# Performance work log

Measured on AMD Instinct MI355X. Metric: run time of the kernel, lower is better.

Reference implementation:

```python
import jax, jax.numpy as jnp
import numpy as np

B, S, D, H, F = 4, 2048, 256, 8, 2  # batch, seq, input_size, heads, mlp factor
EPS = 1e-5


def _ln(x, g, b):
    m = jnp.mean(x, axis=-1, keepdims=True)
    v = jnp.var(x, axis=-1, keepdims=True)
    return (x - m) / jnp.sqrt(v + EPS) * g + b


def setup_inputs() -> dict:
    key = jax.random.key(0)
    ks = jax.random.split(key, 12)
    s = 1.0 / np.sqrt(D)
    return {
        "X":  jax.random.normal(ks[0], (B, S, D), jnp.float32),
        # Wide attention: each of H heads has full [D,D] Q/K/V projections (no bias)
        "Wq": jax.random.uniform(ks[1], (H, D, D), jnp.float32, -s, s),
        "Wk": jax.random.uniform(ks[2], (H, D, D), jnp.float32, -s, s),
        "Wv": jax.random.uniform(ks[3], (H, D, D), jnp.float32, -s, s),
        "Wz": jax.random.uniform(ks[4], (H * D, D), jnp.float32, -1.0 / np.sqrt(H * D), 1.0 / np.sqrt(H * D)),
        "bz": jnp.zeros((D,), jnp.float32),
        "W1": jax.random.uniform(ks[5], (D, F * D), jnp.float32, -s, s),
        "b1": jnp.zeros((F * D,), jnp.float32),
        "W2": jax.random.uniform(ks[6], (F * D, D), jnp.float32, -1.0 / np.sqrt(F * D), 1.0 / np.sqrt(F * D)),
        "b2": jnp.zeros((D,), jnp.float32),
        "g1": jnp.ones((D,), jnp.float32),
        "be1": jnp.zeros((D,), jnp.float32),
        "g2": jnp.ones((D,), jnp.float32),
        "be2": jnp.zeros((D,), jnp.float32),
    }


def reference(X, Wq, Wk, Wv, Wz, bz, W1, b1, W2, b2, g1, be1, g2, be2):
    scale = D ** (-0.25)  # applied to both q and k as in the source
    q = jnp.einsum('bsd,hde->hbse', X, Wq) * scale   # [H,B,S,D]
    k = jnp.einsum('btd,hde->hbte', X, Wk) * scale
    v = jnp.einsum('btd,hde->hbte', X, Wv)
    attn = jax.nn.softmax(jnp.einsum('hbse,hbte->hbst', q, k), axis=-1)  # [H,B,S,S]
    zh = jnp.einsum('hbst,hbte->hbse', attn, v)       # [H,B,S,D]
    # concat heads along feature dim (head order matters for Wz)
    zcat = jnp.transpose(zh, (1, 2, 0, 3)).reshape(B, S, H * D)
    z = zcat @ Wz + bz
    z = _ln(z + X, g1, be1)                            # dropout p=0 -> identity
    z_ff = jnp.maximum(z @ W1 + b1, 0.0) @ W2 + b2
    z = _ln(z_ff + z, g2, be2)
    attn_mean = jnp.mean(attn, axis=0)                 # [B,S,S]
    return z, attn_mean
```

## Files before the change

kernel.cpp:

```cpp
#include <hip/hip_runtime.h>
#include <cstdint>
#include <cstddef>

#define B_  4
#define S_  2048
#define D_  256
#define H_  8
#define FD_ 512
#define N_  (B_*S_)
#define HD_ (H_*D_)
#define EPS 1e-5f

typedef __attribute__((ext_vector_type(8))) short bf16x8;
typedef __attribute__((ext_vector_type(8))) unsigned short u16x8;
typedef __attribute__((ext_vector_type(4))) float f32x4;

__device__ __forceinline__ unsigned short f2bf(float f) {
  union { float f; unsigned u; } x; x.f = f;
  unsigned u = x.u;
  return (unsigned short)((u + 0x7FFFu + ((u >> 16) & 1u)) >> 16);
}
__device__ __forceinline__ float bf2f(unsigned short h) {
  union { unsigned u; float f; } x; x.u = ((unsigned)h) << 16; return x.f;
}

__device__ __forceinline__ void glds16(const void* gptr, void* ldsptr) {
  __builtin_amdgcn_global_load_lds(
      (__attribute__((address_space(1))) void*)gptr,
      (__attribute__((address_space(3))) void*)ldsptr,
      16, 0, 0);
}

__device__ __forceinline__ int sw32(int row, int u) {
  return (row*32 + ((u & 24) | ((u & 7) ^ (row & 7)))) * 8;
}
__device__ __forceinline__ int sw16(int row, int u) {
  return (row*16 + ((u & 8) | ((u & 7) ^ (row & 7)))) * 8;
}

__global__ __launch_bounds__(256) void cast_x_kernel(
    const float* __restrict__ X, unsigned short* __restrict__ Xb)
{
  const size_t i8 = ((size_t)blockIdx.x * 256 + threadIdx.x) * 8;
  float4 a = *(const float4*)&X[i8];
  float4 b = *(const float4*)&X[i8 + 4];
  u16x8 o;
  o[0]=f2bf(a.x); o[1]=f2bf(a.y); o[2]=f2bf(a.z); o[3]=f2bf(a.w);
  o[4]=f2bf(b.x); o[5]=f2bf(b.y); o[6]=f2bf(b.z); o[7]=f2bf(b.w);
  *(u16x8*)&Xb[i8] = o;
}

__global__ __launch_bounds__(256) void prep_w_kernel(
    const float* __restrict__ Wq, const float* __restrict__ Wk,
    const float* __restrict__ Wv, unsigned short* __restrict__ Wt)
{
  __shared__ float tile[64][65];
  const int tid = threadIdx.x;
  const int d0 = blockIdx.x * 64, e0 = blockIdx.y * 64;
  const int w = blockIdx.z;
  const float* src;
  float scale;
  if (w < 8)       { src = Wq + (size_t)w*D_*D_;      scale = 0.25f; }
  else if (w < 16) { src = Wk + (size_t)(w-8)*D_*D_;  scale = 0.25f; }
  else             { src = Wv + (size_t)(w-16)*D_*D_; scale = 1.0f;  }
  {
    int r = tid >> 2, c16 = (tid & 3) * 16;
    const float* s = src + (size_t)(d0 + r)*D_ + e0 + c16;
    #pragma unroll
    for (int u = 0; u < 4; ++u) *(float4*)&tile[r][c16 + u*4] = *(const float4*)(s + u*4);
  }
  __syncthreads();
  {
    int er = tid >> 2, dc = (tid & 3) * 16;
    u16x8 o0, o1;
    #pragma unroll
    for (int j = 0; j < 8; ++j) {
      o0[j] = f2bf(tile[dc + j][er] * scale);
      o1[j] = f2bf(tile[dc + 8 + j][er] * scale);
    }
    unsigned short* dst = Wt + ((size_t)w*D_ + e0 + er)*D_ + d0 + dc;
    *(u16x8*)(dst)     = o0;
    *(u16x8*)(dst + 8) = o1;
  }
}

__global__ __launch_bounds__(256) void tcast_kernel(
    const float* __restrict__ src, unsigned short* __restrict__ dst,
    int R, int C)
{
  __shared__ float tile[64][65];
  const int tid = threadIdx.x;
  const int r0 = blockIdx.x * 64, c0 = blockIdx.y * 64;
  {
    int r = tid >> 2, c16 = (tid & 3) * 16;
    const float* s = src + (size_t)(r0 + r)*C + c0 + c16;
    #pragma unroll
    for (int u = 0; u < 4; ++u) *(float4*)&tile[r][c16 + u*4] = *(const float4*)(s + u*4);
  }
  __syncthreads();
  {
    int cr = tid >> 2, rc = (tid & 3) * 16;
    u16x8 o0, o1;
    #pragma unroll
    for (int j = 0; j < 8; ++j) {
      o0[j] = f2bf(tile[rc + j][cr]);
      o1[j] = f2bf(tile[rc + 8 + j][cr]);
    }
    unsigned short* d = dst + (size_t)(c0 + cr)*R + r0 + rc;
    *(u16x8*)(d)     = o0;
    *(u16x8*)(d + 8) = o1;
  }
}

__global__ __launch_bounds__(256) void qkv_kernel(
    const unsigned short* __restrict__ Xb, const unsigned short* __restrict__ Wt,
    unsigned short* __restrict__ q, unsigned short* __restrict__ k,
    unsigned short* __restrict__ v)
{
  __shared__ unsigned short Xt[64*32*8];
  __shared__ unsigned short Wtile[64*32*8];
  const int tid = threadIdx.x;
  const int w4 = tid >> 6, lane = tid & 63;
  const int c = lane & 15, qd = lane >> 4;
  const int n0 = blockIdx.x * 64;
  const int e0 = blockIdx.y * 64;
  const int w  = blockIdx.z;

  unsigned short* obase;
  if (w < 8)       obase = q + (size_t)w*N_*D_;
  else if (w < 16) obase = k + (size_t)(w-8)*N_*D_;
  else             obase = v + (size_t)(w-16)*N_*D_;

  {
    const char* xg = (const char*)Xb + (size_t)n0*512;
    const char* wg = (const char*)Wt + ((size_t)w*D_ + e0)*512;
    #pragma unroll
    for (int i = 0; i < 8; ++i) {
      int g = w4*8 + i;
      int r = 2*g + (lane >> 5);
      int su = lane & 31;
      int u = (su & 24) | ((su & 7) ^ (r & 7));
      glds16(xg + (size_t)r*512 + u*16, &Xt[g*512]);
      glds16(wg + (size_t)r*512 + u*16, &Wtile[g*512]);
    }
  }
  __syncthreads();

  f32x4 sc[4];
  #pragma unroll
  for (int nc = 0; nc < 4; ++nc) sc[nc] = (f32x4){0.f,0.f,0.f,0.f};
  #pragma unroll
  for (int ks = 0; ks < 8; ++ks) {
    bf16x8 xa = *(const bf16x8*)&Xt[sw32(16*w4 + c, ks*4 + qd)];
    #pragma unroll
    for (int nc = 0; nc < 4; ++nc) {
      bf16x8 bf = *(const bf16x8*)&Wtile[sw32(nc*16 + c, ks*4 + qd)];
      sc[nc] = __builtin_amdgcn_mfma_f32_16x16x32_bf16(xa, bf, sc[nc], 0, 0, 0);
    }
  }
  #pragma unroll
  for (int nc = 0; nc < 4; ++nc)
    #pragma unroll
    for (int r = 0; r < 4; ++r)
      obase[(size_t)(n0 + 16*w4 + qd*4 + r)*D_ + e0 + nc*16 + c] = f2bf(sc[nc][r]);
}

__global__ __launch_bounds__(256) void vtrans_kernel(
    const unsigned short* __restrict__ vb, unsigned short* __restrict__ vT)
{
  __shared__ unsigned short tile[64][72];
  const int tid = threadIdx.x;
  const int t0 = blockIdx.x * 64, e0 = blockIdx.y * 64;
  const int h = blockIdx.z >> 2, b = blockIdx.z & 3;
  const size_t in_base = (size_t)h*N_*D_ + (size_t)b*S_*D_;
  {
    int r = tid >> 2, c16 = (tid & 3) * 16;
    const unsigned short* src = vb + in_base + (size_t)(t0 + r)*D_ + e0 + c16;
    *(u16x8*)&tile[r][c16]     = *(const u16x8*)(src);
    *(u16x8*)&tile[r][c16 + 8] = *(const u16x8*)(src + 8);
  }
  __syncthreads();
  {
    int er = tid >> 2, tt = (tid & 3) * 16;
    u16x8 o0, o1;
    #pragma unroll
    for (int j = 0; j < 8; ++j) { o0[j] = tile[tt+j][er]; o1[j] = tile[tt+8+j][er]; }
    unsigned short* dst = vT + ((size_t)(h*4 + b)*D_ + e0 + er)*S_ + t0 + tt;
    *(u16x8*)(dst)     = o0;
    *(u16x8*)(dst + 8) = o1;
  }
}

__global__ __launch_bounds__(256, 2) void attn_ol_kernel(
    const unsigned short* __restrict__ qb, const unsigned short* __restrict__ kb,
    const unsigned short* __restrict__ vT, unsigned short* __restrict__ zcatb,
    float* __restrict__ Lws)
{
  __shared__ unsigned short Kt[2][32*32*8];
  __shared__ unsigned short Vt[2][16*544];
  const int tid = threadIdx.x;
  const int w = tid >> 6, lane = tid & 63;
  const int c = lane & 15, qd = lane >> 4;
  const int wg = blockIdx.x;
  const int xcd = wg & 7;
  const int slot = wg >> 3;
  const int j = slot & 15;
  const int gg = slot >> 4;
  const int g = gg*8 + xcd;
  const int h = g >> 2, b = g & 3;
  const int s0 = j * 128;

  const size_t qkbase = (size_t)h*N_*D_ + (size_t)b*S_*D_;

  bf16x8 qa[2][8];
  #pragma unroll
  for (int mi = 0; mi < 2; ++mi) {
    const unsigned short* qrow = qb + qkbase + (size_t)(s0 + 32*w + 16*mi + c)*D_ + qd*8;
    #pragma unroll
    for (int ks = 0; ks < 8; ++ks) qa[mi][ks] = *(const bf16x8*)(qrow + ks*32);
  }

  f32x4 o[2][16];
  #pragma unroll
  for (int mi = 0; mi < 2; ++mi)
    #pragma unroll
    for (int i = 0; i < 16; ++i) o[mi][i] = (f32x4){0.f,0.f,0.f,0.f};
  float Lp[2] = {0.f, 0.f};

  const char* kB = (const char*)(kb + qkbase);
  const char* vB = (const char*)(vT + (size_t)(h*4 + b)*D_*S_);

  #define STAGE_OL(kt_, bi_)                                                   \
    {                                                                          \
      _Pragma("unroll")                                                        \
      for (int i = 0; i < 4; ++i) {                                            \
        int gq = w*4 + i;                                                      \
        int r = 2*gq + (lane >> 5);                                            \
        int Lg = ((r >> 2) & 3)*8 + (r >> 4)*4 + (r & 3);                      \
        int su = lane & 31;                                                    \
        int u = (su & 24) | ((su & 7) ^ (r & 7));                              \
        glds16(kB + ((size_t)(kt_)*32 + Lg)*512 + u*16, &Kt[bi_][gq*512]);     \
      }                                                                        \
      _Pragma("unroll")                                                        \
      for (int i = 0; i < 4; ++i) {                                            \
        int gq = w*4 + i;                                                      \
        int e = gq*16 + (lane >> 2);                                           \
        int qv = (lane & 3) ^ ((lane >> 3) & 3);                               \
        glds16(vB + (size_t)e*4096 + (size_t)(kt_)*64 + qv*16, &Vt[bi_][gq*544]);\
      }                                                                        \
    }

  STAGE_OL(0, 0);

  for (int kt = 0; kt < 64; ++kt) {
    const int bi = kt & 1;
    __syncthreads();
    if (kt + 1 < 64) STAGE_OL(kt + 1, bi ^ 1);

    f32x4 sc[2][2];
    #pragma unroll
    for (int mi = 0; mi < 2; ++mi)
      #pragma unroll
      for (int nc = 0; nc < 2; ++nc) sc[mi][nc] = (f32x4){0.f,0.f,0.f,0.f};
    #pragma unroll
    for (int ks = 0; ks < 8; ++ks) {
      bf16x8 kf0 = *(const bf16x8*)&Kt[bi][sw32(c,      ks*4 + qd)];
      bf16x8 kf1 = *(const bf16x8*)&Kt[bi][sw32(16 + c, ks*4 + qd)];
      #pragma unroll
      for (int mi = 0; mi < 2; ++mi) {
        sc[mi][0] = __builtin_amdgcn_mfma_f32_16x16x32_bf16(kf0, qa[mi][ks], sc[mi][0], 0, 0, 0);
        sc[mi][1] = __builtin_amdgcn_mfma_f32_16x16x32_bf16(kf1, qa[mi][ks], sc[mi][1], 0, 0, 0);
      }
    }
    bf16x8 pa[2];
    #pragma unroll
    for (int mi = 0; mi < 2; ++mi) {
      float ex[2][4];
      #pragma unroll
      for (int nc = 0; nc < 2; ++nc)
        #pragma unroll
        for (int r = 0; r < 4; ++r) {
          float p = __expf(sc[mi][nc][r]);
          ex[nc][r] = p;
          Lp[mi] += p;
        }
      union { unsigned u[4]; bf16x8 v; } cv;
      asm("v_cvt_pk_bf16_f32 %0, %1, %2" : "=v"(cv.u[0]) : "v"(ex[0][0]), "v"(ex[0][1]));
      asm("v_cvt_pk_bf16_f32 %0, %1, %2" : "=v"(cv.u[1]) : "v"(ex[0][2]), "v"(ex[0][3]));
      asm("v_cvt_pk_bf16_f32 %0, %1, %2" : "=v"(cv.u[2]) : "v"(ex[1][0]), "v"(ex[1][1]));
      asm("v_cvt_pk_bf16_f32 %0, %1, %2" : "=v"(cv.u[3]) : "v"(ex[1][2]), "v"(ex[1][3]));
      pa[mi] = cv.v;
    }
    #pragma unroll
    for (int ec = 0; ec < 16; ++ec) {
      bf16x8 vf = *(const bf16x8*)&Vt[bi][ec*544 + c*32 + (qd ^ ((c >> 1) & 3))*8];
      o[0][ec] = __builtin_amdgcn_mfma_f32_16x16x32_bf16(pa[0], vf, o[0][ec], 0, 0, 0);
      o[1][ec] = __builtin_amdgcn_mfma_f32_16x16x32_bf16(pa[1], vf, o[1][ec], 0, 0, 0);
    }
  }

  #pragma unroll
  for (int mi = 0; mi < 2; ++mi) {
    float L = Lp[mi];
    L += __shfl_xor(L, 16);
    L += __shfl_xor(L, 32);
    if (qd == 0)
      Lws[(size_t)h*N_ + b*S_ + s0 + 32*w + 16*mi + c] = L;
    float il[4];
    #pragma unroll
    for (int r = 0; r < 4; ++r)
      il[r] = 1.0f / __shfl(L, (lane & 48) | (qd*4 + r));
    #pragma unroll
    for (int ec = 0; ec < 16; ++ec)
      #pragma unroll
      for (int r = 0; r < 4; ++r)
        zcatb[(size_t)(b*S_ + s0 + 32*w + 16*mi + qd*4 + r)*HD_ + h*D_ + ec*16 + c] =
            f2bf(o[mi][ec][r] * il[r]);
  }
  #undef STAGE_OL
}

__global__ __launch_bounds__(256, 2) void attn_mean_kernel(
    const unsigned short* __restrict__ qb, const unsigned short* __restrict__ kb,
    const float* __restrict__ Lws, float* __restrict__ out_attn)
{
  __shared__ unsigned short Kt[2][64*32*8];
  const int tid = threadIdx.x;
  const int w = tid >> 6, lane = tid & 63;
  const int c = lane & 15, qd = lane >> 4;
  const int wg = blockIdx.x;
  const int xcd = wg & 7;
  const int slot = wg >> 3;
  const int j = slot & 15;
  const int ggg = slot >> 4;
  const int g = ggg*8 + xcd;
  const int b = g >> 5;
  const int t0 = (g & 31) * 64;
  const int s0 = j * 128;

  float am[2][4][4] = {};

  #define STAGE_AM(h_, bi_)                                                    \
    {                                                                          \
      const char* kB = (const char*)(kb + (size_t)(h_)*N_*D_ + (size_t)b*S_*D_);\
      _Pragma("unroll")                                                        \
      for (int i = 0; i < 8; ++i) {                                            \
        int gq = w*8 + i;                                                      \
        int r = 2*gq + (lane >> 5);                                            \
        int su = lane & 31;                                                    \
        int u = (su & 24) | ((su & 7) ^ (r & 7));                              \
        glds16(kB + ((size_t)t0 + r)*512 + u*16, &Kt[bi_][gq*512]);            \
      }                                                                        \
    }

  STAGE_AM(0, 0);

  bf16x8 qa[2][8];
  #pragma unroll
  for (int mi = 0; mi < 2; ++mi) {
    const unsigned short* qrow = qb + (size_t)b*S_*D_ + (size_t)(s0 + 32*w + 16*mi + c)*D_ + qd*8;
    #pragma unroll
    for (int ks = 0; ks < 8; ++ks) qa[mi][ks] = *(const bf16x8*)(qrow + ks*32);
  }

  for (int h = 0; h < 8; ++h) {
    const int bi = h & 1;
    __syncthreads();
    if (h + 1 < 8) STAGE_AM(h + 1, bi ^ 1);

    float il[2][4];
    #pragma unroll
    for (int mi = 0; mi < 2; ++mi)
      #pragma unroll
      for (int r = 0; r < 4; ++r)
        il[mi][r] = 0.125f / Lws[(size_t)h*N_ + b*S_ + s0 + 32*w + 16*mi + qd*4 + r];

    bf16x8 qn[2][8];
    if (h + 1 < 8) {
      const size_t basen = (size_t)(h+1)*N_*D_ + (size_t)b*S_*D_;
      #pragma unroll
      for (int mi = 0; mi < 2; ++mi) {
        const unsigned short* qrow = qb + basen + (size_t)(s0 + 32*w + 16*mi + c)*D_ + qd*8;
        #pragma unroll
        for (int ks = 0; ks < 8; ++ks) qn[mi][ks] = *(const bf16x8*)(qrow + ks*32);
      }
    }

    f32x4 sc[2][4];
    #pragma unroll
    for (int mi = 0; mi < 2; ++mi)
      #pragma unroll
      for (int nc = 0; nc < 4; ++nc) sc[mi][nc] = (f32x4){0.f,0.f,0.f,0.f};
    #pragma unroll
    for (int ks = 0; ks < 8; ++ks) {
      #pragma unroll
      for (int nc = 0; nc < 4; ++nc) {
        bf16x8 kf = *(const bf16x8*)&Kt[bi][sw32(nc*16 + c, ks*4 + qd)];
        sc[0][nc] = __builtin_amdgcn_mfma_f32_16x16x32_bf16(qa[0][ks], kf, sc[0][nc], 0, 0, 0);
        sc[1][nc] = __builtin_amdgcn_mfma_f32_16x16x32_bf16(qa[1][ks], kf, sc[1][nc], 0, 0, 0);
      }
    }
    #pragma unroll
    for (int mi = 0; mi < 2; ++mi)
      #pragma unroll
      for (int nc = 0; nc < 4; ++nc)
        #pragma unroll
        for (int r = 0; r < 4; ++r)
          am[mi][nc][r] += __expf(sc[mi][nc][r]) * il[mi][r];

    if (h + 1 < 8) {
      #pragma unroll
      for (int mi = 0; mi < 2; ++mi)
        #pragma unroll
        for (int ks = 0; ks < 8; ++ks) qa[mi][ks] = qn[mi][ks];
    }
  }
  #pragma unroll
  for (int mi = 0; mi < 2; ++mi)
    #pragma unroll
    for (int nc = 0; nc < 4; ++nc)
      #pragma unroll
      for (int r = 0; r < 4; ++r)
        out_attn[(size_t)(b*S_ + s0 + 32*w + 16*mi + qd*4 + r)*S_ + t0 + nc*16 + c] =
            am[mi][nc][r];
  #undef STAGE_AM
}

__global__ __launch_bounds__(256) void wz_ln1_kernel(
    const unsigned short* __restrict__ zcatb, const unsigned short* __restrict__ Wzt,
    const float* __restrict__ bz, const float* __restrict__ X,
    const float* __restrict__ g1, const float* __restrict__ be1,
    unsigned short* __restrict__ z1b)
{
  __shared__ unsigned short At[32*16*8];
  __shared__ unsigned short Wt2[256*16*8];
  __shared__ float redS[2][32], redQ[2][32];
  const int tid = threadIdx.x;
  const int w4 = tid >> 6, lane = tid & 63;
  const int c = lane & 15, qd = lane >> 4;
  const int n0 = blockIdx.x * 32;
  const int msub = w4 & 1, ehalf = w4 >> 1;

  f32x4 acc[8];
  #pragma unroll
  for (int nc = 0; nc < 8; ++nc) acc[nc] = (f32x4){0.f,0.f,0.f,0.f};

  for (int kc = 0; kc < 16; ++kc) {
    {
      const char* ab = (const char*)zcatb + (size_t)n0*4096 + (size_t)kc*256;
      #pragma unroll
      for (int i = 0; i < 2; ++i) {
        int g = w4*2 + i;
        int r = g*4 + (lane >> 4);
        int su = lane & 15;
        int u = (su & 8) | ((su & 7) ^ (r & 7));
        glds16(ab + (size_t)r*4096 + u*16, &At[g*512]);
      }
      const char* wb = (const char*)Wzt + (size_t)kc*256;
      #pragma unroll
      for (int i = 0; i < 16; ++i) {
        int g = w4*16 + i;
        int e = g*4 + (lane >> 4);
        int su = lane & 15;
        int u = (su & 8) | ((su & 7) ^ (e & 7));
        glds16(wb + (size_t)e*4096 + u*16, &Wt2[g*512]);
      }
    }
    __syncthreads();
    #pragma unroll
    for (int ks = 0; ks < 4; ++ks) {
      bf16x8 a = *(const bf16x8*)&At[sw16(msub*16 + c, ks*4 + qd)];
      #pragma unroll
      for (int nc = 0; nc < 8; ++nc) {
        bf16x8 bv = *(const bf16x8*)&Wt2[sw16(ehalf*128 + nc*16 + c, ks*4 + qd)];
        acc[nc] = __builtin_amdgcn_mfma_f32_16x16x32_bf16(a, bv, acc[nc], 0, 0, 0);
      }
    }
    __syncthreads();
  }

  float vals[8][4];
  float sum_[4] = {0.f,0.f,0.f,0.f}, sq_[4] = {0.f,0.f,0.f,0.f};
  #pragma unroll
  for (int nc = 0; nc < 8; ++nc) {
    int e = ehalf*128 + nc*16 + c;
    #pragma unroll
    for (int r = 0; r < 4; ++r) {
      int n = n0 + msub*16 + qd*4 + r;
      float v = acc[nc][r] + bz[e] + X[(size_t)n*D_ + e];
      vals[nc][r] = v;
      sum_[r] += v; sq_[r] += v*v;
    }
  }
  #pragma unroll
  for (int off = 1; off < 16; off <<= 1) {
    #pragma unroll
    for (int r = 0; r < 4; ++r) {
      sum_[r] += __shfl_xor(sum_[r], off);
      sq_[r]  += __shfl_xor(sq_[r],  off);
    }
  }
  if (c == 0) {
    #pragma unroll
    for (int r = 0; r < 4; ++r) {
      redS[ehalf][msub*16 + qd*4 + r] = sum_[r];
      redQ[ehalf][msub*16 + qd*4 + r] = sq_[r];
    }
  }
  __syncthreads();
  #pragma unroll
  for (int r = 0; r < 4; ++r) {
    int lr = msub*16 + qd*4 + r;
    float Sv = redS[0][lr] + redS[1][lr];
    float Qv = redQ[0][lr] + redQ[1][lr];
    float mean = Sv * (1.0f/D_);
    float var  = Qv * (1.0f/D_) - mean*mean;
    float rstd = rsqrtf(var + EPS);
    int n = n0 + lr;
    #pragma unroll
    for (int nc = 0; nc < 8; ++nc) {
      int e = ehalf*128 + nc*16 + c;
      z1b[(size_t)n*D_ + e] = f2bf((vals[nc][r] - mean)*rstd*g1[e] + be1[e]);
    }
  }
}

__global__ __launch_bounds__(256) void mlp1_kernel(
    const unsigned short* __restrict__ z1b, const unsigned short* __restrict__ W1t,
    const float* __restrict__ b1, unsigned short* __restrict__ hbuf)
{
  __shared__ unsigned short At[64*32*8];
  __shared__ unsigned short Bt[64*32*8];
  const int tid = threadIdx.x;
  const int w4 = tid >> 6, lane = tid & 63;
  const int c = lane & 15, qd = lane >> 4;
  const int n0 = blockIdx.x * 64;
  const int f0 = blockIdx.y * 64;

  {
    const char* ag = (const char*)z1b + (size_t)n0*512;
    const char* bg = (const char*)W1t + (size_t)f0*512;
    #pragma unroll
    for (int i = 0; i < 8; ++i) {
      int g = w4*8 + i;
      int r = 2*g + (lane >> 5);
      int su = lane & 31;
      int u = (su & 24) | ((su & 7) ^ (r & 7));
      glds16(ag + (size_t)r*512 + u*16, &At[g*512]);
      glds16(bg + (size_t)r*512 + u*16, &Bt[g*512]);
    }
  }
  __syncthreads();

  f32x4 sc[4];
  #pragma unroll
  for (int nc = 0; nc < 4; ++nc) sc[nc] = (f32x4){0.f,0.f,0.f,0.f};
  #pragma unroll
  for (int ks = 0; ks < 8; ++ks) {
    bf16x8 xa = *(const bf16x8*)&At[sw32(16*w4 + c, ks*4 + qd)];
    #pragma unroll
    for (int nc = 0; nc < 4; ++nc) {
      bf16x8 bf = *(const bf16x8*)&Bt[sw32(nc*16 + c, ks*4 + qd)];
      sc[nc] = __builtin_amdgcn_mfma_f32_16x16x32_bf16(xa, bf, sc[nc], 0, 0, 0);
    }
  }
  #pragma unroll
  for (int nc = 0; nc < 4; ++nc) {
    int f = f0 + nc*16 + c;
    float bias = b1[f];
    #pragma unroll
    for (int r = 0; r < 4; ++r)
      hbuf[(size_t)(n0 + 16*w4 + qd*4 + r)*FD_ + f] = f2bf(fmaxf(sc[nc][r] + bias, 0.f));
  }
}

__global__ __launch_bounds__(256) void mlp2_kernel(
    const unsigned short* __restrict__ hbuf, const unsigned short* __restrict__ W2t,
    const float* __restrict__ b2, const unsigned short* __restrict__ z1b,
    const float* __restrict__ g2, const float* __restrict__ be2,
    float* __restrict__ out)
{
  __shared__ unsigned short At[32*16*8];
  __shared__ unsigned short Wt2[256*16*8];
  __shared__ float redS[2][32], redQ[2][32];
  const int tid = threadIdx.x;
  const int w4 = tid >> 6, lane = tid & 63;
  const int c = lane & 15, qd = lane >> 4;
  const int n0 = blockIdx.x * 32;
  const int msub = w4 & 1, ehalf = w4 >> 1;

  f32x4 acc[8];
  #pragma unroll
  for (int nc = 0; nc < 8; ++nc) acc[nc] = (f32x4){0.f,0.f,0.f,0.f};

  for (int kc = 0; kc < 4; ++kc) {
    {
      const char* ab = (const char*)hbuf + (size_t)n0*1024 + (size_t)kc*256;
      #pragma unroll
      for (int i = 0; i < 2; ++i) {
        int g = w4*2 + i;
        int r = g*4 + (lane >> 4);
        int su = lane & 15;
        int u = (su & 8) | ((su & 7) ^ (r & 7));
        glds16(ab + (size_t)r*1024 + u*16, &At[g*512]);
      }
      const char* wb = (const char*)W2t + (size_t)kc*256;
      #pragma unroll
      for (int i = 0; i < 16; ++i) {
        int g = w4*16 + i;
        int e = g*4 + (lane >> 4);
        int su = lane & 15;
        int u = (su & 8) | ((su & 7) ^ (e & 7));
        glds16(wb + (size_t)e*1024 + u*16, &Wt2[g*512]);
      }
    }
    __syncthreads();
    #pragma unroll
    for (int ks = 0; ks < 4; ++ks) {
      bf16x8 a = *(const bf16x8*)&At[sw16(msub*16 + c, ks*4 + qd)];
      #pragma unroll
      for (int nc = 0; nc < 8; ++nc) {
        bf16x8 bv = *(const bf16x8*)&Wt2[sw16(ehalf*128 + nc*16 + c, ks*4 + qd)];
        acc[nc] = __builtin_amdgcn_mfma_f32_16x16x32_bf16(a, bv, acc[nc], 0, 0, 0);
      }
    }
    __syncthreads();
  }

  float vals[8][4];
  float sum_[4] = {0.f,0.f,0.f,0.f}, sq_[4] = {0.f,0.f,0.f,0.f};
  #pragma unroll
  for (int nc = 0; nc < 8; ++nc) {
    int e = ehalf*128 + nc*16 + c;
    #pragma unroll
    for (int r = 0; r < 4; ++r) {
      int n = n0 + msub*16 + qd*4 + r;
      float v = acc[nc][r] + b2[e] + bf2f(z1b[(size_t)n*D_ + e]);
      vals[nc][r] = v;
      sum_[r] += v; sq_[r] += v*v;
    }
  }
  #pragma unroll
  for (int off = 1; off < 16; off <<= 1) {
    #pragma unroll
    for (int r = 0; r < 4; ++r) {
      sum_[r] += __shfl_xor(sum_[r], off);
      sq_[r]  += __shfl_xor(sq_[r],  off);
    }
  }
  if (c == 0) {
    #pragma unroll
    for (int r = 0; r < 4; ++r) {
      redS[ehalf][msub*16 + qd*4 + r] = sum_[r];
      redQ[ehalf][msub*16 + qd*4 + r] = sq_[r];
    }
  }
  __syncthreads();
  #pragma unroll
  for (int r = 0; r < 4; ++r) {
    int lr = msub*16 + qd*4 + r;
    float Sv = redS[0][lr] + redS[1][lr];
    float Qv = redQ[0][lr] + redQ[1][lr];
    float mean = Sv * (1.0f/D_);
    float var  = Qv * (1.0f/D_) - mean*mean;
    float rstd = rsqrtf(var + EPS);
    int n = n0 + lr;
    #pragma unroll
    for (int nc = 0; nc < 8; ++nc) {
      int e = ehalf*128 + nc*16 + c;
      out[(size_t)n*D_ + e] = (vals[nc][r] - mean)*rstd*g2[e] + be2[e];
    }
  }
}

extern "C" void kernel_launch(void* const* d_in, const int* in_sizes, int n_in,
                              void* d_out, int out_size, void* d_ws, size_t ws_size,
                              hipStream_t stream)
{
  (void)in_sizes; (void)n_in; (void)out_size; (void)ws_size;
  const float* X   = (const float*)d_in[0];
  const float* Wq  = (const float*)d_in[1];
  const float* Wk  = (const float*)d_in[2];
  const float* Wv  = (const float*)d_in[3];
  const float* Wz  = (const float*)d_in[4];
  const float* bz  = (const float*)d_in[5];
  const float* W1  = (const float*)d_in[6];
  const float* b1  = (const float*)d_in[7];
  const float* W2  = (const float*)d_in[8];
  const float* b2  = (const float*)d_in[9];
  const float* g1  = (const float*)d_in[10];
  const float* be1 = (const float*)d_in[11];
  const float* g2  = (const float*)d_in[12];
  const float* be2 = (const float*)d_in[13];

  char* p = (char*)d_ws;
  unsigned short* Xbb  = (unsigned short*)p; p += (size_t)N_*D_*2;
  unsigned short* Wtb  = (unsigned short*)p; p += (size_t)24*D_*D_*2;
  unsigned short* Wztb = (unsigned short*)p; p += (size_t)D_*HD_*2;
  unsigned short* W1tb = (unsigned short*)p; p += (size_t)FD_*D_*2;
  unsigned short* W2tb = (unsigned short*)p; p += (size_t)D_*FD_*2;
  unsigned short* qbuf = (unsigned short*)p; p += (size_t)H_*N_*D_*2;
  unsigned short* kbuf = (unsigned short*)p; p += (size_t)H_*N_*D_*2;
  unsigned short* vbuf = (unsigned short*)p; p += (size_t)H_*N_*D_*2;
  unsigned short* vTb  = (unsigned short*)p; p += (size_t)H_*N_*D_*2;
  float* Lws   = (float*)p; p += (size_t)H_*N_*4;
  unsigned short* zcatb = (unsigned short*)p; p += (size_t)N_*HD_*2;
  unsigned short* z1b   = (unsigned short*)p; p += (size_t)N_*D_*2;
  unsigned short* hbuf  = (unsigned short*)p;

  float* out_z    = (float*)d_out;
  float* out_attn = out_z + (size_t)N_*D_;

  cast_x_kernel<<<N_*D_/(256*8), 256, 0, stream>>>(X, Xbb);

  dim3 gW(4, 4, 24);
  prep_w_kernel<<<gW, 256, 0, stream>>>(Wq, Wk, Wv, Wtb);

  { dim3 g(HD_/64, D_/64);  tcast_kernel<<<g, 256, 0, stream>>>(Wz, Wztb, HD_, D_); }
  { dim3 g(D_/64, FD_/64);  tcast_kernel<<<g, 256, 0, stream>>>(W1, W1tb, D_, FD_); }
  { dim3 g(FD_/64, D_/64);  tcast_kernel<<<g, 256, 0, stream>>>(W2, W2tb, FD_, D_); }

  dim3 gA(N_/64, D_/64, 24);
  qkv_kernel<<<gA, 256, 0, stream>>>(Xbb, Wtb, qbuf, kbuf, vbuf);

  dim3 gT(S_/64, D_/64, H_*B_);
  vtrans_kernel<<<gT, 256, 0, stream>>>(vbuf, vTb);

  attn_ol_kernel<<<512, 256, 0, stream>>>(qbuf, kbuf, vTb, zcatb, Lws);

  attn_mean_kernel<<<2048, 256, 0, stream>>>(qbuf, kbuf, Lws, out_attn);

  wz_ln1_kernel<<<N_/32, 256, 0, stream>>>(zcatb, Wztb, bz, X, g1, be1, z1b);

  dim3 gM1(N_/64, FD_/64);
  mlp1_kernel<<<gM1, 256, 0, stream>>>(z1b, W1tb, b1, hbuf);

  mlp2_kernel<<<N_/32, 256, 0, stream>>>(hbuf, W2tb, b2, z1b, g2, be2, out_z);
}
```

Measured before the change: 533.8 us.

## Load K and Q fragments directly from global memory instead of LDS staging

```diff
diff --git a/kernel.cpp b/kernel.cpp
--- a/kernel.cpp
+++ b/kernel.cpp
@@ -196,7 +196,6 @@
     const unsigned short* __restrict__ vT, unsigned short* __restrict__ zcatb,
     float* __restrict__ Lws)
 {
-  __shared__ unsigned short Kt[2][32*32*8];
   __shared__ unsigned short Vt[2][16*544];
   const int tid = threadIdx.x;
   const int w = tid >> 6, lane = tid & 63;
@@ -230,17 +229,11 @@
   const char* kB = (const char*)(kb + qkbase);
   const char* vB = (const char*)(vT + (size_t)(h*4 + b)*D_*S_);
 
+  const int rowb0 = (((c >> 2) & 3)*8 + (c & 3))*512 + qd*16;
+  const int rowb1 = rowb0 + 4*512;
+
   #define STAGE_OL(kt_, bi_)                                                   \
     {                                                                          \
-      _Pragma("unroll")                                                        \
-      for (int i = 0; i < 4; ++i) {                                            \
-        int gq = w*4 + i;                                                      \
-        int r = 2*gq + (lane >> 5);                                            \
-        int Lg = ((r >> 2) & 3)*8 + (r >> 4)*4 + (r & 3);                      \
-        int su = lane & 31;                                                    \
-        int u = (su & 24) | ((su & 7) ^ (r & 7));                              \
-        glds16(kB + ((size_t)(kt_)*32 + Lg)*512 + u*16, &Kt[bi_][gq*512]);     \
-      }                                                                        \
       _Pragma("unroll")                                                        \
       for (int i = 0; i < 4; ++i) {                                            \
         int gq = w*4 + i;                                                      \
@@ -257,6 +250,7 @@
     __syncthreads();
     if (kt + 1 < 64) STAGE_OL(kt + 1, bi ^ 1);
 
+    const char* ktb = kB + (size_t)kt*16384;
     f32x4 sc[2][2];
     #pragma unroll
     for (int mi = 0; mi < 2; ++mi)
@@ -264,8 +258,8 @@
       for (int nc = 0; nc < 2; ++nc) sc[mi][nc] = (f32x4){0.f,0.f,0.f,0.f};
     #pragma unroll
     for (int ks = 0; ks < 8; ++ks) {
-      bf16x8 kf0 = *(const bf16x8*)&Kt[bi][sw32(c,      ks*4 + qd)];
-      bf16x8 kf1 = *(const bf16x8*)&Kt[bi][sw32(16 + c, ks*4 + qd)];
+      bf16x8 kf0 = *(const bf16x8*)(ktb + rowb0 + ks*64);
+      bf16x8 kf1 = *(const bf16x8*)(ktb + rowb1 + ks*64);
       #pragma unroll
       for (int mi = 0; mi < 2; ++mi) {
         sc[mi][0] = __builtin_amdgcn_mfma_f32_16x16x32_bf16(kf0, qa[mi][ks], sc[mi][0], 0, 0, 0);
@@ -320,11 +314,10 @@
   #undef STAGE_OL
 }
 
-__global__ __launch_bounds__(256, 2) void attn_mean_kernel(
+__global__ __launch_bounds__(256, 4) void attn_mean_kernel(
     const unsigned short* __restrict__ qb, const unsigned short* __restrict__ kb,
     const float* __restrict__ Lws, float* __restrict__ out_attn)
 {
-  __shared__ unsigned short Kt[2][64*32*8];
   const int tid = threadIdx.x;
   const int w = tid >> 6, lane = tid & 63;
   const int c = lane & 15, qd = lane >> 4;
@@ -340,33 +333,13 @@
 
   float am[2][4][4] = {};
 
-  #define STAGE_AM(h_, bi_)                                                    \
-    {                                                                          \
-      const char* kB = (const char*)(kb + (size_t)(h_)*N_*D_ + (size_t)b*S_*D_);\
-      _Pragma("unroll")                                                        \
-      for (int i = 0; i < 8; ++i) {                                            \
-        int gq = w*8 + i;                                                      \
-        int r = 2*gq + (lane >> 5);                                            \
-        int su = lane & 31;                                                    \
-        int u = (su & 24) | ((su & 7) ^ (r & 7));                              \
-        glds16(kB + ((size_t)t0 + r)*512 + u*16, &Kt[bi_][gq*512]);            \
-      }                                                                        \
-    }
-
-  STAGE_AM(0, 0);
-
-  bf16x8 qa[2][8];
-  #pragma unroll
-  for (int mi = 0; mi < 2; ++mi) {
-    const unsigned short* qrow = qb + (size_t)b*S_*D_ + (size_t)(s0 + 32*w + 16*mi + c)*D_ + qd*8;
-    #pragma unroll
-    for (int ks = 0; ks < 8; ++ks) qa[mi][ks] = *(const bf16x8*)(qrow + ks*32);
-  }
+  const char* qBase = (const char*)qb + ((size_t)b*S_ + s0 + 32*w + c)*512 + qd*16;
+  const char* kBase = (const char*)kb + ((size_t)b*S_ + t0 + c)*512 + qd*16;
 
   for (int h = 0; h < 8; ++h) {
-    const int bi = h & 1;
-    __syncthreads();
-    if (h + 1 < 8) STAGE_AM(h + 1, bi ^ 1);
+    const size_t hoff = (size_t)h*N_*D_*2;
+    const char* qh = qBase + hoff;
+    const char* kh = kBase + hoff;
 
     float il[2][4];
     #pragma unroll
@@ -375,17 +348,6 @@
       for (int r = 0; r < 4; ++r)
         il[mi][r] = 0.125f / Lws[(size_t)h*N_ + b*S_ + s0 + 32*w + 16*mi + qd*4 + r];
 
-    bf16x8 qn[2][8];
-    if (h + 1 < 8) {
-      const size_t basen = (size_t)(h+1)*N_*D_ + (size_t)b*S_*D_;
-      #pragma unroll
-      for (int mi = 0; mi < 2; ++mi) {
-        const unsigned short* qrow = qb + basen + (size_t)(s0 + 32*w + 16*mi + c)*D_ + qd*8;
-        #pragma unroll
-        for (int ks = 0; ks < 8; ++ks) qn[mi][ks] = *(const bf16x8*)(qrow + ks*32);
-      }
-    }
-
     f32x4 sc[2][4];
     #pragma unroll
     for (int mi = 0; mi < 2; ++mi)
@@ -393,11 +355,13 @@
       for (int nc = 0; nc < 4; ++nc) sc[mi][nc] = (f32x4){0.f,0.f,0.f,0.f};
     #pragma unroll
     for (int ks = 0; ks < 8; ++ks) {
+      bf16x8 qa0 = *(const bf16x8*)(qh + ks*64);
+      bf16x8 qa1 = *(const bf16x8*)(qh + 16*512 + ks*64);
       #pragma unroll
       for (int nc = 0; nc < 4; ++nc) {
-        bf16x8 kf = *(const bf16x8*)&Kt[bi][sw32(nc*16 + c, ks*4 + qd)];
-        sc[0][nc] = __builtin_amdgcn_mfma_f32_16x16x32_bf16(qa[0][ks], kf, sc[0][nc], 0, 0, 0);
-        sc[1][nc] = __builtin_amdgcn_mfma_f32_16x16x32_bf16(qa[1][ks], kf, sc[1][nc], 0, 0, 0);
+        bf16x8 kf = *(const bf16x8*)(kh + nc*16*512 + ks*64);
+        sc[0][nc] = __builtin_amdgcn_mfma_f32_16x16x32_bf16(qa0, kf, sc[0][nc], 0, 0, 0);
+        sc[1][nc] = __builtin_amdgcn_mfma_f32_16x16x32_bf16(qa1, kf, sc[1][nc], 0, 0, 0);
       }
     }
     #pragma unroll
@@ -407,13 +371,6 @@
         #pragma unroll
         for (int r = 0; r < 4; ++r)
           am[mi][nc][r] += __expf(sc[mi][nc][r]) * il[mi][r];
-
-    if (h + 1 < 8) {
-      #pragma unroll
-      for (int mi = 0; mi < 2; ++mi)
-        #pragma unroll
-        for (int ks = 0; ks < 8; ++ks) qa[mi][ks] = qn[mi][ks];
-    }
   }
   #pragma unroll
   for (int mi = 0; mi < 2; ++mi)
@@ -423,7 +380,6 @@
       for (int r = 0; r < 4; ++r)
         out_attn[(size_t)(b*S_ + s0 + 32*w + 16*mi + qd*4 + r)*S_ + t0 + nc*16 + c] =
             am[mi][nc][r];
-  #undef STAGE_AM
 }
 
 __global__ __launch_bounds__(256) void wz_ln1_kernel(
```

Result: slower. 881.6 us (+65.2%).

## Single-buffer K tile and drop Q prefetch in attn_mean to raise occupancy

Applied to the files above, without the earlier changes.

```diff
diff --git a/kernel.cpp b/kernel.cpp
--- a/kernel.cpp
+++ b/kernel.cpp
@@ -320,11 +320,11 @@
   #undef STAGE_OL
 }
 
-__global__ __launch_bounds__(256, 2) void attn_mean_kernel(
+__global__ __launch_bounds__(256, 4) void attn_mean_kernel(
     const unsigned short* __restrict__ qb, const unsigned short* __restrict__ kb,
     const float* __restrict__ Lws, float* __restrict__ out_attn)
 {
-  __shared__ unsigned short Kt[2][64*32*8];
+  __shared__ unsigned short Kt[64*32*8];
   const int tid = threadIdx.x;
   const int w = tid >> 6, lane = tid & 63;
   const int c = lane & 15, qd = lane >> 4;
@@ -340,7 +340,7 @@
 
   float am[2][4][4] = {};
 
-  #define STAGE_AM(h_, bi_)                                                    \
+  #define STAGE_AM(h_)                                                         \
     {                                                                          \
       const char* kB = (const char*)(kb + (size_t)(h_)*N_*D_ + (size_t)b*S_*D_);\
       _Pragma("unroll")                                                        \
@@ -349,25 +349,21 @@
         int r = 2*gq + (lane >> 5);                                            \
         int su = lane & 31;                                                    \
         int u = (su & 24) | ((su & 7) ^ (r & 7));                              \
-        glds16(kB + ((size_t)t0 + r)*512 + u*16, &Kt[bi_][gq*512]);            \
+        glds16(kB + ((size_t)t0 + r)*512 + u*16, &Kt[gq*512]);                 \
       }                                                                        \
     }
 
-  STAGE_AM(0, 0);
-
-  bf16x8 qa[2][8];
-  #pragma unroll
-  for (int mi = 0; mi < 2; ++mi) {
-    const unsigned short* qrow = qb + (size_t)b*S_*D_ + (size_t)(s0 + 32*w + 16*mi + c)*D_ + qd*8;
-    #pragma unroll
-    for (int ks = 0; ks < 8; ++ks) qa[mi][ks] = *(const bf16x8*)(qrow + ks*32);
-  }
+  STAGE_AM(0);
 
   for (int h = 0; h < 8; ++h) {
-    const int bi = h & 1;
-    __syncthreads();
-    if (h + 1 < 8) STAGE_AM(h + 1, bi ^ 1);
-
+    bf16x8 qa[2][8];
+    const size_t base = (size_t)h*N_*D_ + (size_t)b*S_*D_;
+    #pragma unroll
+    for (int mi = 0; mi < 2; ++mi) {
+      const unsigned short* qrow = qb + base + (size_t)(s0 + 32*w + 16*mi + c)*D_ + qd*8;
+      #pragma unroll
+      for (int ks = 0; ks < 8; ++ks) qa[mi][ks] = *(const bf16x8*)(qrow + ks*32);
+    }
     float il[2][4];
     #pragma unroll
     for (int mi = 0; mi < 2; ++mi)
@@ -375,16 +371,7 @@
       for (int r = 0; r < 4; ++r)
         il[mi][r] = 0.125f / Lws[(size_t)h*N_ + b*S_ + s0 + 32*w + 16*mi + qd*4 + r];
 
-    bf16x8 qn[2][8];
-    if (h + 1 < 8) {
-      const size_t basen = (size_t)(h+1)*N_*D_ + (size_t)b*S_*D_;
-      #pragma unroll
-      for (int mi = 0; mi < 2; ++mi) {
-        const unsigned short* qrow = qb + basen + (size_t)(s0 + 32*w + 16*mi + c)*D_ + qd*8;
-        #pragma unroll
-        for (int ks = 0; ks < 8; ++ks) qn[mi][ks] = *(const bf16x8*)(qrow + ks*32);
-      }
-    }
+    __syncthreads();
 
     f32x4 sc[2][4];
     #pragma unroll
@@ -395,11 +382,17 @@
     for (int ks = 0; ks < 8; ++ks) {
       #pragma unroll
       for (int nc = 0; nc < 4; ++nc) {
-        bf16x8 kf = *(const bf16x8*)&Kt[bi][sw32(nc*16 + c, ks*4 + qd)];
+        bf16x8 kf = *(const bf16x8*)&Kt[sw32(nc*16 + c, ks*4 + qd)];
         sc[0][nc] = __builtin_amdgcn_mfma_f32_16x16x32_bf16(qa[0][ks], kf, sc[0][nc], 0, 0, 0);
         sc[1][nc] = __builtin_amdgcn_mfma_f32_16x16x32_bf16(qa[1][ks], kf, sc[1][nc], 0, 0, 0);
       }
     }
+
+    if (h + 1 < 8) {
+      __syncthreads();
+      STAGE_AM(h + 1);
+    }
+
     #pragma unroll
     for (int mi = 0; mi < 2; ++mi)
       #pragma unroll
@@ -407,13 +400,6 @@
         #pragma unroll
         for (int r = 0; r < 4; ++r)
           am[mi][nc][r] += __expf(sc[mi][nc][r]) * il[mi][r];
-
-    if (h + 1 < 8) {
-      #pragma unroll
-      for (int mi = 0; mi < 2; ++mi)
-        #pragma unroll
-        for (int ks = 0; ks < 8; ++ks) qa[mi][ks] = qn[mi][ks];
-    }
   }
   #pragma unroll
   for (int mi = 0; mi < 2; ++mi)
```

Result: slower. 699.2 us (+31.0%).

## Merge attention-mean and Wz+LayerNorm kernels into one branch-dispatched launch

Applied to the files above, without the earlier changes.

```diff
diff --git a/kernel.cpp b/kernel.cpp
--- a/kernel.cpp
+++ b/kernel.cpp
@@ -320,207 +320,208 @@
   #undef STAGE_OL
 }
 
-__global__ __launch_bounds__(256, 2) void attn_mean_kernel(
+#define FATSMEM (73728 + 512)
+__global__ __launch_bounds__(256, 2) void attn_mean_wz_kernel(
     const unsigned short* __restrict__ qb, const unsigned short* __restrict__ kb,
-    const float* __restrict__ Lws, float* __restrict__ out_attn)
-{
-  __shared__ unsigned short Kt[2][64*32*8];
-  const int tid = threadIdx.x;
-  const int w = tid >> 6, lane = tid & 63;
-  const int c = lane & 15, qd = lane >> 4;
-  const int wg = blockIdx.x;
-  const int xcd = wg & 7;
-  const int slot = wg >> 3;
-  const int j = slot & 15;
-  const int ggg = slot >> 4;
-  const int g = ggg*8 + xcd;
-  const int b = g >> 5;
-  const int t0 = (g & 31) * 64;
-  const int s0 = j * 128;
-
-  float am[2][4][4] = {};
-
-  #define STAGE_AM(h_, bi_)                                                    \
-    {                                                                          \
-      const char* kB = (const char*)(kb + (size_t)(h_)*N_*D_ + (size_t)b*S_*D_);\
-      _Pragma("unroll")                                                        \
-      for (int i = 0; i < 8; ++i) {                                            \
-        int gq = w*8 + i;                                                      \
-        int r = 2*gq + (lane >> 5);                                            \
-        int su = lane & 31;                                                    \
-        int u = (su & 24) | ((su & 7) ^ (r & 7));                              \
-        glds16(kB + ((size_t)t0 + r)*512 + u*16, &Kt[bi_][gq*512]);            \
-      }                                                                        \
-    }
-
-  STAGE_AM(0, 0);
-
-  bf16x8 qa[2][8];
-  #pragma unroll
-  for (int mi = 0; mi < 2; ++mi) {
-    const unsigned short* qrow = qb + (size_t)b*S_*D_ + (size_t)(s0 + 32*w + 16*mi + c)*D_ + qd*8;
-    #pragma unroll
-    for (int ks = 0; ks < 8; ++ks) qa[mi][ks] = *(const bf16x8*)(qrow + ks*32);
-  }
-
-  for (int h = 0; h < 8; ++h) {
-    const int bi = h & 1;
-    __syncthreads();
-    if (h + 1 < 8) STAGE_AM(h + 1, bi ^ 1);
-
-    float il[2][4];
-    #pragma unroll
-    for (int mi = 0; mi < 2; ++mi)
-      #pragma unroll
-      for (int r = 0; r < 4; ++r)
-        il[mi][r] = 0.125f / Lws[(size_t)h*N_ + b*S_ + s0 + 32*w + 16*mi + qd*4 + r];
-
-    bf16x8 qn[2][8];
-    if (h + 1 < 8) {
-      const size_t basen = (size_t)(h+1)*N_*D_ + (size_t)b*S_*D_;
-      #pragma unroll
-      for (int mi = 0; mi < 2; ++mi) {
-        const unsigned short* qrow = qb + basen + (size_t)(s0 + 32*w + 16*mi + c)*D_ + qd*8;
-        #pragma unroll
-        for (int ks = 0; ks < 8; ++ks) qn[mi][ks] = *(const bf16x8*)(qrow + ks*32);
-      }
-    }
-
-    f32x4 sc[2][4];
-    #pragma unroll
-    for (int mi = 0; mi < 2; ++mi)
-      #pragma unroll
-      for (int nc = 0; nc < 4; ++nc) sc[mi][nc] = (f32x4){0.f,0.f,0.f,0.f};
-    #pragma unroll
-    for (int ks = 0; ks < 8; ++ks) {
-      #pragma unroll
-      for (int nc = 0; nc < 4; ++nc) {
-        bf16x8 kf = *(const bf16x8*)&Kt[bi][sw32(nc*16 + c, ks*4 + qd)];
-        sc[0][nc] = __builtin_amdgcn_mfma_f32_16x16x32_bf16(qa[0][ks], kf, sc[0][nc], 0, 0, 0);
-        sc[1][nc] = __builtin_amdgcn_mfma_f32_16x16x32_bf16(qa[1][ks], kf, sc[1][nc], 0, 0, 0);
-      }
-    }
-    #pragma unroll
-    for (int mi = 0; mi < 2; ++mi)
-      #pragma unroll
-      for (int nc = 0; nc < 4; ++nc)
-        #pragma unroll
-        for (int r = 0; r < 4; ++r)
-          am[mi][nc][r] += __expf(sc[mi][nc][r]) * il[mi][r];
-
-    if (h + 1 < 8) {
-      #pragma unroll
-      for (int mi = 0; mi < 2; ++mi)
-        #pragma unroll
-        for (int ks = 0; ks < 8; ++ks) qa[mi][ks] = qn[mi][ks];
-    }
-  }
-  #pragma unroll
-  for (int mi = 0; mi < 2; ++mi)
-    #pragma unroll
-    for (int nc = 0; nc < 4; ++nc)
-      #pragma unroll
-      for (int r = 0; r < 4; ++r)
-        out_attn[(size_t)(b*S_ + s0 + 32*w + 16*mi + qd*4 + r)*S_ + t0 + nc*16 + c] =
-            am[mi][nc][r];
-  #undef STAGE_AM
-}
-
-__global__ __launch_bounds__(256) void wz_ln1_kernel(
+    const float* __restrict__ Lws, float* __restrict__ out_attn,
     const unsigned short* __restrict__ zcatb, const unsigned short* __restrict__ Wzt,
     const float* __restrict__ bz, const float* __restrict__ X,
     const float* __restrict__ g1, const float* __restrict__ be1,
     unsigned short* __restrict__ z1b)
 {
-  __shared__ unsigned short At[32*16*8];
-  __shared__ unsigned short Wt2[256*16*8];
-  __shared__ float redS[2][32], redQ[2][32];
+  __shared__ __align__(16) char smem[FATSMEM];
   const int tid = threadIdx.x;
-  const int w4 = tid >> 6, lane = tid & 63;
+  const int w = tid >> 6, lane = tid & 63;
   const int c = lane & 15, qd = lane >> 4;
-  const int n0 = blockIdx.x * 32;
-  const int msub = w4 & 1, ehalf = w4 >> 1;
-
-  f32x4 acc[8];
-  #pragma unroll
-  for (int nc = 0; nc < 8; ++nc) acc[nc] = (f32x4){0.f,0.f,0.f,0.f};
-
-  for (int kc = 0; kc < 16; ++kc) {
-    {
-      const char* ab = (const char*)zcatb + (size_t)n0*4096 + (size_t)kc*256;
-      #pragma unroll
-      for (int i = 0; i < 2; ++i) {
-        int g = w4*2 + i;
-        int r = g*4 + (lane >> 4);
-        int su = lane & 15;
-        int u = (su & 8) | ((su & 7) ^ (r & 7));
-        glds16(ab + (size_t)r*4096 + u*16, &At[g*512]);
-      }
-      const char* wb = (const char*)Wzt + (size_t)kc*256;
-      #pragma unroll
-      for (int i = 0; i < 16; ++i) {
-        int g = w4*16 + i;
-        int e = g*4 + (lane >> 4);
-        int su = lane & 15;
-        int u = (su & 8) | ((su & 7) ^ (e & 7));
-        glds16(wb + (size_t)e*4096 + u*16, &Wt2[g*512]);
-      }
-    }
-    __syncthreads();
-    #pragma unroll
-    for (int ks = 0; ks < 4; ++ks) {
-      bf16x8 a = *(const bf16x8*)&At[sw16(msub*16 + c, ks*4 + qd)];
-      #pragma unroll
-      for (int nc = 0; nc < 8; ++nc) {
-        bf16x8 bv = *(const bf16x8*)&Wt2[sw16(ehalf*128 + nc*16 + c, ks*4 + qd)];
-        acc[nc] = __builtin_amdgcn_mfma_f32_16x16x32_bf16(a, bv, acc[nc], 0, 0, 0);
-      }
-    }
-    __syncthreads();
-  }
-
-  float vals[8][4];
-  float sum_[4] = {0.f,0.f,0.f,0.f}, sq_[4] = {0.f,0.f,0.f,0.f};
-  #pragma unroll
-  for (int nc = 0; nc < 8; ++nc) {
-    int e = ehalf*128 + nc*16 + c;
-    #pragma unroll
-    for (int r = 0; r < 4; ++r) {
-      int n = n0 + msub*16 + qd*4 + r;
-      float v = acc[nc][r] + bz[e] + X[(size_t)n*D_ + e];
-      vals[nc][r] = v;
-      sum_[r] += v; sq_[r] += v*v;
-    }
-  }
-  #pragma unroll
-  for (int off = 1; off < 16; off <<= 1) {
-    #pragma unroll
-    for (int r = 0; r < 4; ++r) {
-      sum_[r] += __shfl_xor(sum_[r], off);
-      sq_[r]  += __shfl_xor(sq_[r],  off);
-    }
-  }
-  if (c == 0) {
-    #pragma unroll
-    for (int r = 0; r < 4; ++r) {
-      redS[ehalf][msub*16 + qd*4 + r] = sum_[r];
-      redQ[ehalf][msub*16 + qd*4 + r] = sq_[r];
-    }
-  }
-  __syncthreads();
-  #pragma unroll
-  for (int r = 0; r < 4; ++r) {
-    int lr = msub*16 + qd*4 + r;
-    float Sv = redS[0][lr] + redS[1][lr];
-    float Qv = redQ[0][lr] + redQ[1][lr];
-    float mean = Sv * (1.0f/D_);
-    float var  = Qv * (1.0f/D_) - mean*mean;
-    float rstd = rsqrtf(var + EPS);
-    int n = n0 + lr;
+  const int bid = blockIdx.x;
+
+  if (bid < 2048) {
+    unsigned short (*Kt)[64*32*8] = (unsigned short (*)[64*32*8])smem;
+    const int xcd = bid & 7;
+    const int slot = bid >> 3;
+    const int j = slot & 15;
+    const int ggg = slot >> 4;
+    const int g = ggg*8 + xcd;
+    const int b = g >> 5;
+    const int t0 = (g & 31) * 64;
+    const int s0 = j * 128;
+
+    float am[2][4][4] = {};
+
+    #define STAGE_AM(h_, bi_)                                                  \
+      {                                                                        \
+        const char* kB = (const char*)(kb + (size_t)(h_)*N_*D_ + (size_t)b*S_*D_);\
+        _Pragma("unroll")                                                      \
+        for (int i = 0; i < 8; ++i) {                                          \
+          int gq = w*8 + i;                                                    \
+          int r = 2*gq + (lane >> 5);                                          \
+          int su = lane & 31;                                                  \
+          int u = (su & 24) | ((su & 7) ^ (r & 7));                            \
+          glds16(kB + ((size_t)t0 + r)*512 + u*16, &Kt[bi_][gq*512]);          \
+        }                                                                      \
+      }
+
+    STAGE_AM(0, 0);
+
+    bf16x8 qa[2][8];
+    #pragma unroll
+    for (int mi = 0; mi < 2; ++mi) {
+      const unsigned short* qrow = qb + (size_t)b*S_*D_ + (size_t)(s0 + 32*w + 16*mi + c)*D_ + qd*8;
+      #pragma unroll
+      for (int ks = 0; ks < 8; ++ks) qa[mi][ks] = *(const bf16x8*)(qrow + ks*32);
+    }
+
+    for (int h = 0; h < 8; ++h) {
+      const int bi = h & 1;
+      __syncthreads();
+      if (h + 1 < 8) STAGE_AM(h + 1, bi ^ 1);
+
+      float il[2][4];
+      #pragma unroll
+      for (int mi = 0; mi < 2; ++mi)
+        #pragma unroll
+        for (int r = 0; r < 4; ++r)
+          il[mi][r] = 0.125f / Lws[(size_t)h*N_ + b*S_ + s0 + 32*w + 16*mi + qd*4 + r];
+
+      bf16x8 qn[2][8];
+      if (h + 1 < 8) {
+        const size_t basen = (size_t)(h+1)*N_*D_ + (size_t)b*S_*D_;
+        #pragma unroll
+        for (int mi = 0; mi < 2; ++mi) {
+          const unsigned short* qrow = qb + basen + (size_t)(s0 + 32*w + 16*mi + c)*D_ + qd*8;
+          #pragma unroll
+          for (int ks = 0; ks < 8; ++ks) qn[mi][ks] = *(const bf16x8*)(qrow + ks*32);
+        }
+      }
+
+      f32x4 sc[2][4];
+      #pragma unroll
+      for (int mi = 0; mi < 2; ++mi)
+        #pragma unroll
+        for (int nc = 0; nc < 4; ++nc) sc[mi][nc] = (f32x4){0.f,0.f,0.f,0.f};
+      #pragma unroll
+      for (int ks = 0; ks < 8; ++ks) {
+        #pragma unroll
+        for (int nc = 0; nc < 4; ++nc) {
+          bf16x8 kf = *(const bf16x8*)&Kt[bi][sw32(nc*16 + c, ks*4 + qd)];
+          sc[0][nc] = __builtin_amdgcn_mfma_f32_16x16x32_bf16(qa[0][ks], kf, sc[0][nc], 0, 0, 0);
+          sc[1][nc] = __builtin_amdgcn_mfma_f32_16x16x32_bf16(qa[1][ks], kf, sc[1][nc], 0, 0, 0);
+        }
+      }
+      #pragma unroll
+      for (int mi = 0; mi < 2; ++mi)
+        #pragma unroll
+        for (int nc = 0; nc < 4; ++nc)
+          #pragma unroll
+          for (int r = 0; r < 4; ++r)
+            am[mi][nc][r] += __expf(sc[mi][nc][r]) * il[mi][r];
+
+      if (h + 1 < 8) {
+        #pragma unroll
+        for (int mi = 0; mi < 2; ++mi)
+          #pragma unroll
+          for (int ks = 0; ks < 8; ++ks) qa[mi][ks] = qn[mi][ks];
+      }
+    }
+    #pragma unroll
+    for (int mi = 0; mi < 2; ++mi)
+      #pragma unroll
+      for (int nc = 0; nc < 4; ++nc)
+        #pragma unroll
+        for (int r = 0; r < 4; ++r)
+          out_attn[(size_t)(b*S_ + s0 + 32*w + 16*mi + qd*4 + r)*S_ + t0 + nc*16 + c] =
+              am[mi][nc][r];
+    #undef STAGE_AM
+  } else {
+    unsigned short* At  = (unsigned short*)smem;
+    unsigned short* Wt2 = (unsigned short*)(smem + 8192);
+    float (*redS)[32] = (float (*)[32])(smem + 73728);
+    float (*redQ)[32] = (float (*)[32])(smem + 73728 + 256);
+    const int n0 = (bid - 2048) * 32;
+    const int w4 = w;
+    const int msub = w4 & 1, ehalf = w4 >> 1;
+
+    f32x4 acc[8];
+    #pragma unroll
+    for (int nc = 0; nc < 8; ++nc) acc[nc] = (f32x4){0.f,0.f,0.f,0.f};
+
+    for (int kc = 0; kc < 16; ++kc) {
+      {
+        const char* ab = (const char*)zcatb + (size_t)n0*4096 + (size_t)kc*256;
+        #pragma unroll
+        for (int i = 0; i < 2; ++i) {
+          int g = w4*2 + i;
+          int r = g*4 + (lane >> 4);
+          int su = lane & 15;
+          int u = (su & 8) | ((su & 7) ^ (r & 7));
+          glds16(ab + (size_t)r*4096 + u*16, &At[g*512]);
+        }
+        const char* wb = (const char*)Wzt + (size_t)kc*256;
+        #pragma unroll
+        for (int i = 0; i < 16; ++i) {
+          int g = w4*16 + i;
+          int e = g*4 + (lane >> 4);
+          int su = lane & 15;
+          int u = (su & 8) | ((su & 7) ^ (e & 7));
+          glds16(wb + (size_t)e*4096 + u*16, &Wt2[g*512]);
+        }
+      }
+      __syncthreads();
+      #pragma unroll
+      for (int ks = 0; ks < 4; ++ks) {
+        bf16x8 a = *(const bf16x8*)&At[sw16(msub*16 + c, ks*4 + qd)];
+        #pragma unroll
+        for (int nc = 0; nc < 8; ++nc) {
+          bf16x8 bv = *(const bf16x8*)&Wt2[sw16(ehalf*128 + nc*16 + c, ks*4 + qd)];
+          acc[nc] = __builtin_amdgcn_mfma_f32_16x16x32_bf16(a, bv, acc[nc], 0, 0, 0);
+        }
+      }
+      __syncthreads();
+    }
+
+    float vals[8][4];
+    float sum_[4] = {0.f,0.f,0.f,0.f}, sq_[4] = {0.f,0.f,0.f,0.f};
     #pragma unroll
     for (int nc = 0; nc < 8; ++nc) {
       int e = ehalf*128 + nc*16 + c;
-      z1b[(size_t)n*D_ + e] = f2bf((vals[nc][r] - mean)*rstd*g1[e] + be1[e]);
+      #pragma unroll
+      for (int r = 0; r < 4; ++r) {
+        int n = n0 + msub*16 + qd*4 + r;
+        float v = acc[nc][r] + bz[e] + X[(size_t)n*D_ + e];
+        vals[nc][r] = v;
+        sum_[r] += v; sq_[r] += v*v;
+      }
+    }
+    #pragma unroll
+    for (int off = 1; off < 16; off <<= 1) {
+      #pragma unroll
+      for (int r = 0; r < 4; ++r) {
+        sum_[r] += __shfl_xor(sum_[r], off);
+        sq_[r]  += __shfl_xor(sq_[r],  off);
+      }
+    }
+    if (c == 0) {
+      #pragma unroll
+      for (int r = 0; r < 4; ++r) {
+        redS[ehalf][msub*16 + qd*4 + r] = sum_[r];
+        redQ[ehalf][msub*16 + qd*4 + r] = sq_[r];
+      }
+    }
+    __syncthreads();
+    #pragma unroll
+    for (int r = 0; r < 4; ++r) {
+      int lr = msub*16 + qd*4 + r;
+      float Sv = redS[0][lr] + redS[1][lr];
+      float Qv = redQ[0][lr] + redQ[1][lr];
+      float mean = Sv * (1.0f/D_);
+      float var  = Qv * (1.0f/D_) - mean*mean;
+      float rstd = rsqrtf(var + EPS);
+      int n = n0 + lr;
+      #pragma unroll
+      for (int nc = 0; nc < 8; ++nc) {
+        int e = ehalf*128 + nc*16 + c;
+        z1b[(size_t)n*D_ + e] = f2bf((vals[nc][r] - mean)*rstd*g1[e] + be1[e]);
+      }
     }
   }
 }
@@ -728,9 +729,8 @@
 
   attn_ol_kernel<<<512, 256, 0, stream>>>(qbuf, kbuf, vTb, zcatb, Lws);
 
-  attn_mean_kernel<<<2048, 256, 0, stream>>>(qbuf, kbuf, Lws, out_attn);
-
-  wz_ln1_kernel<<<N_/32, 256, 0, stream>>>(zcatb, Wztb, bz, X, g1, be1, z1b);
+  attn_mean_wz_kernel<<<2304, 256, 0, stream>>>(
+      qbuf, kbuf, Lws, out_attn, zcatb, Wztb, bz, X, g1, be1, z1b);
 
   dim3 gM1(N_/64, FD_/64);
   mlp1_kernel<<<gM1, 256, 0, stream>>>(z1b, W1tb, b1, hbuf);
```

Result: no change. 527.0 us (-1.3%).
